# Kernel tuning notes

Measured on AMD Instinct MI355X. Metric: run time of the kernel, lower is better.

## Reference

```python
import jax, jax.numpy as jnp
import numpy as np

N = 50000
E = 1600000
IN_C, HID_C, OUT_C, EDGE_D = 128, 64, 64, 32
NEG_SLOPE = 0.2


def _add_self_loops(edge_index, edge_attr, n):
    # PyG add_self_loops with fill_value='mean': loop attr = mean of incoming edge attrs per node
    src, dst = edge_index[0], edge_index[1]
    attr_sum = jax.ops.segment_sum(edge_attr, dst, num_segments=n)          # [N, D]
    cnt = jax.ops.segment_sum(jnp.ones((edge_attr.shape[0],), edge_attr.dtype), dst, num_segments=n)
    loop_attr = attr_sum / jnp.maximum(cnt, 1.0)[:, None]                   # [N, D]
    loop = jnp.arange(n, dtype=src.dtype)
    src = jnp.concatenate([src, loop])
    dst = jnp.concatenate([dst, loop])
    edge_attr = jnp.concatenate([edge_attr, loop_attr], axis=0)
    return src, dst, edge_attr


def gat_conv(x, edge_index, edge_attr, W, We, att_src, att_dst, att_edge, bias, n):
    # heads=1, concat=True (PyG defaults); att_* have shape [1, C]
    src, dst, ea = _add_self_loops(edge_index, edge_attr, n)
    h = x @ W                                   # [N, C]
    a_src = jnp.sum(h * att_src, axis=-1)       # [N]
    a_dst = jnp.sum(h * att_dst, axis=-1)       # [N]
    he = ea @ We                                # [E+N, C]
    a_edge = jnp.sum(he * att_edge, axis=-1)    # [E+N]
    alpha = a_src[src] + a_dst[dst] + a_edge
    alpha = jax.nn.leaky_relu(alpha, NEG_SLOPE)
    # segment softmax over destination nodes (every node has a self-loop)
    m = jax.ops.segment_max(alpha, dst, num_segments=n)
    alpha = jnp.exp(alpha - m[dst])
    denom = jax.ops.segment_sum(alpha, dst, num_segments=n)
    alpha = alpha / (denom[dst] + 1e-16)
    out = jax.ops.segment_sum(alpha[:, None] * h[src], dst, num_segments=n)  # [N, C]
    return out + bias


def setup_inputs() -> dict:
    key = jax.random.key(0)
    ks = jax.random.split(key, 12)
    def g(k, shape, scale=1.0):
        return jax.random.normal(k, shape, dtype=jnp.float32) * scale
    x = g(ks[0], (N, IN_C))
    edge_index = jax.random.randint(ks[1], (2, E), 0, N, dtype=jnp.int64)
    edge_attr = g(ks[2], (E, EDGE_D))
    s1 = 1.0 / np.sqrt(IN_C)
    s2 = 1.0 / np.sqrt(HID_C)
    se = 1.0 / np.sqrt(EDGE_D)
    return {
        "x": x, "edge_index": edge_index, "edge_attr": edge_attr,
        "W1": g(ks[3], (IN_C, HID_C), s1), "We1": g(ks[4], (EDGE_D, HID_C), se),
        "att_src1": g(ks[5], (1, HID_C), s2), "att_dst1": g(ks[6], (1, HID_C), s2),
        "att_edge1": g(ks[7], (1, HID_C), s2), "b1": jnp.zeros((HID_C,), jnp.float32),
        "W2": g(ks[8], (HID_C, OUT_C), s2), "We2": g(ks[9], (EDGE_D, OUT_C), se),
        "att_src2": g(ks[10], (1, OUT_C), s2), "att_dst2": g(ks[11], (1, OUT_C), s2),
        "att_edge2": g(jax.random.fold_in(key, 99), (1, OUT_C), s2),
        "b2": jnp.zeros((OUT_C,), jnp.float32),
    }


def reference(x, edge_index, edge_attr,
              W1, We1, att_src1, att_dst1, att_edge1, b1,
              W2, We2, att_src2, att_dst2, att_edge2, b2):
    h = gat_conv(x, edge_index, edge_attr, W1, We1, att_src1, att_dst1, att_edge1, b1, N)
    h = jax.nn.relu(h)
    # F.dropout(p=0.1, training=self.training): identity in eval mode
    out = gat_conv(h, edge_index, edge_attr, W2, We2, att_src2, att_dst2, att_edge2, b2, N)
    return out
```

## Files before the change

### kernel.cpp

```cpp
#include <hip/hip_runtime.h>
#include <hip/hip_bf16.h>

__device__ __forceinline__ unsigned f2bf_rne(float f) {
    unsigned u = __float_as_uint(f);
    u += 0x7FFFu + ((u >> 16) & 1u);
    return u >> 16;
}
__device__ __forceinline__ float bf_lo(unsigned p) { return __uint_as_float(p << 16); }
__device__ __forceinline__ float bf_hi(unsigned p) { return __uint_as_float(p & 0xFFFF0000u); }
template <int I> __device__ __forceinline__ float bfsel(unsigned p) {
    return (I == 0) ? bf_lo(p) : bf_hi(p);
}

__global__ __launch_bounds__(256)
void init_kernel(int* __restrict__ cnt, int n,
                 const float* __restrict__ We1, const float* __restrict__ ae1v,
                 const float* __restrict__ We2, const float* __restrict__ ae2v,
                 float* __restrict__ we1, float* __restrict__ we2) {
    int i = blockIdx.x * 256 + threadIdx.x;
    if (i < n) cnt[i] = 0;
    if (blockIdx.x == 0 && threadIdx.x >= 64 && threadIdx.x < 128) {
        int t = threadIdx.x - 64;
        const float* W = (t < 32) ? We1 : We2;
        const float* a = (t < 32) ? ae1v : ae2v;
        float* o       = (t < 32) ? we1 : we2;
        int k = t & 31;
        float s = 0.f;
        for (int c = 0; c < 64; ++c) s += W[k * 64 + c] * a[c];
        o[k] = s;
    }
}

__global__ __launch_bounds__(256)
void edge_pass_kernel(const float4* __restrict__ ea, const int* __restrict__ eidx,
                      const float* __restrict__ we1g, const float* __restrict__ we2g,
                      int* __restrict__ cnt, uint2* __restrict__ pack8,
                      unsigned* __restrict__ meta, int E) {
    int tid = threadIdx.x;
    int q = tid & 7;
    int e = blockIdx.x * 32 + (tid >> 3);
    if (e >= E) return;
    float4 w1 = ((const float4*)we1g)[q];
    float4 w2 = ((const float4*)we2g)[q];
    float4 v = ea[(size_t)e * 8 + q];
    float a1 = v.x * w1.x + v.y * w1.y + v.z * w1.z + v.w * w1.w;
    float a2 = v.x * w2.x + v.y * w2.y + v.z * w2.z + v.w * w2.w;
#pragma unroll
    for (int off = 1; off < 8; off <<= 1) {
        a1 += __shfl_xor(a1, off, 64);
        a2 += __shfl_xor(a2, off, 64);
    }
    if (q == 0) {
        int src = eidx[e];
        int dst = eidx[E + e];
        int rk = atomicAdd(&cnt[dst], 1);
        pack8[e] = make_uint2((unsigned)src, f2bf_rne(a1) | (f2bf_rne(a2) << 16));
        meta[e] = ((unsigned)rk << 16) | (unsigned)dst;
    }
}

__global__ __launch_bounds__(256)
void scanA_kernel(const int* __restrict__ cnt, int* __restrict__ bsum, int n) {
    int idx = blockIdx.x * 256 + threadIdx.x;
    int v = (idx < n) ? cnt[idx] : 0;
#pragma unroll
    for (int off = 32; off >= 1; off >>= 1) v += __shfl_xor(v, off, 64);
    __shared__ int ws[4];
    int lane = threadIdx.x & 63, wid = threadIdx.x >> 6;
    if (lane == 0) ws[wid] = v;
    __syncthreads();
    if (threadIdx.x == 0) bsum[blockIdx.x] = ws[0] + ws[1] + ws[2] + ws[3];
}

__global__ __launch_bounds__(256)
void scanC_kernel(const int* __restrict__ cnt, const int* __restrict__ bsum,
                  int* __restrict__ row_ptr, int n, int E) {
    __shared__ int ws[4];
    __shared__ int woff[4];
    __shared__ int bws[4];
    int lane = threadIdx.x & 63, wid = threadIdx.x >> 6;
    int partial = 0;
    for (int j = threadIdx.x; j < blockIdx.x; j += 256) partial += bsum[j];
#pragma unroll
    for (int off = 32; off >= 1; off >>= 1) partial += __shfl_xor(partial, off, 64);
    if (lane == 0) bws[wid] = partial;
    __syncthreads();
    int boff = bws[0] + bws[1] + bws[2] + bws[3];
    int idx = blockIdx.x * 256 + threadIdx.x;
    int v = (idx < n) ? cnt[idx] : 0;
    int s = v;
#pragma unroll
    for (int off = 1; off < 64; off <<= 1) {
        int t = __shfl_up(s, off, 64);
        if (lane >= off) s += t;
    }
    if (lane == 63) ws[wid] = s;
    __syncthreads();
    if (threadIdx.x == 0) {
        int run = 0;
        for (int w = 0; w < 4; ++w) { int t = ws[w]; woff[w] = run; run += t; }
    }
    __syncthreads();
    if (idx < n) row_ptr[idx] = boff + woff[wid] + s - v;
    if (idx == 0) row_ptr[n] = E;
}

__global__ __launch_bounds__(256)
void scatter_kernel(const uint2* __restrict__ pack8, const unsigned* __restrict__ meta,
                    const int* __restrict__ row_ptr, uint2* __restrict__ s_rec, int E) {
    int e = blockIdx.x * 256 + threadIdx.x;
    if (e >= E) return;
    unsigned m = meta[e];
    int dst = (int)(m & 0xFFFFu);
    int rk  = (int)(m >> 16);
    s_rec[row_ptr[dst] + rk] = pack8[e];
}

template <int INC>
__global__ __launch_bounds__(256)
void gemm_kernel(const float* __restrict__ X, const float* __restrict__ W,
                 const float* __restrict__ asv, const float* __restrict__ adv,
                 __hip_bfloat16* __restrict__ H, float* __restrict__ a_src,
                 float* __restrict__ a_dst, int n) {
    constexpr int LDW = INC + 4;
    __shared__ float Wl[64 * LDW];
    for (int t = threadIdx.x; t < INC * 64; t += 256) {
        int k = t >> 6, c = t & 63;
        Wl[c * LDW + k] = W[t];
    }
    __syncthreads();
    int wid = threadIdx.x >> 6, lane = threadIdx.x & 63;
    int i = blockIdx.x * 4 + wid;
    if (i >= n) return;
    const float4* xr = (const float4*)(X + (size_t)i * INC);
    const float4* wr = (const float4*)(Wl + lane * LDW);
    float acc = 0.f;
#pragma unroll
    for (int k4 = 0; k4 < INC / 4; ++k4) {
        float4 xv = xr[k4];
        float4 wv = wr[k4];
        acc += xv.x * wv.x + xv.y * wv.y + xv.z * wv.z + xv.w * wv.w;
    }
    H[(size_t)i * 64 + lane] = __float2bfloat16(acc);
    float s = acc * asv[lane];
    float d = acc * adv[lane];
#pragma unroll
    for (int off = 32; off >= 1; off >>= 1) {
        s += __shfl_xor(s, off, 64);
        d += __shfl_xor(d, off, 64);
    }
    if (lane == 0) { a_src[i] = s; a_dst[i] = d; }
}

__device__ __forceinline__ float4 bf4_to_f4(ushort4 u) {
    float4 f;
    f.x = __uint_as_float((unsigned)u.x << 16);
    f.y = __uint_as_float((unsigned)u.y << 16);
    f.z = __uint_as_float((unsigned)u.z << 16);
    f.w = __uint_as_float((unsigned)u.w << 16);
    return f;
}

template <int AEIDX, bool RELU, bool FUSE_GEMM2>
__global__ __launch_bounds__(256)
void agg_fused_kernel(const int* __restrict__ row_ptr, const uint2* __restrict__ s_rec,
                      const float* __restrict__ a_srcv, const float* __restrict__ a_dstv,
                      const ushort4* __restrict__ H4, const float* __restrict__ bias,
                      float* __restrict__ out,
                      const float* __restrict__ W2, const float* __restrict__ as2v,
                      const float* __restrict__ ad2v, __hip_bfloat16* __restrict__ H2,
                      float* __restrict__ a_src2, float* __restrict__ a_dst2, int n) {
    __shared__ uint2 wl[4][128];
    __shared__ float4 rowl[4][16];
    int wid = threadIdx.x >> 6, lane = threadIdx.x & 63;
    int i = blockIdx.x * 4 + wid;
    if (i >= n) return;
    int start = row_ptr[i], end = row_ptr[i + 1];
    int deg = end - start;
    float adst = a_dstv[i];

    float w0 = 0.f, w1 = 0.f;
    int src0 = 0, src1 = 0;
    float aeloc = 0.f, dloc = 0.f;
    {
        int j = start + lane;
        if (j < end) {
            uint2 r = s_rec[j];
            float ae = bfsel<AEIDX>(r.y);
            src0 = (int)r.x;
            float a = a_srcv[src0] + adst + ae;
            a = a > 0.f ? a : 0.2f * a;
            w0 = __expf(a);
            aeloc += ae; dloc += w0;
        }
    }
    if (deg > 64) {
        int j = start + 64 + lane;
        if (j < end) {
            uint2 r = s_rec[j];
            float ae = bfsel<AEIDX>(r.y);
            src1 = (int)r.x;
            float a = a_srcv[src1] + adst + ae;
            a = a > 0.f ? a : 0.2f * a;
            w1 = __expf(a);
            aeloc += ae; dloc += w1;
        }
    }
    for (int base = start + 128; base < end; base += 64) {
        int j = base + lane;
        if (j < end) {
            uint2 r = s_rec[j];
            float ae = bfsel<AEIDX>(r.y);
            int s = (int)r.x;
            float a = a_srcv[s] + adst + ae;
            a = a > 0.f ? a : 0.2f * a;
            aeloc += ae; dloc += __expf(a);
        }
    }
#pragma unroll
    for (int off = 32; off >= 1; off >>= 1) {
        aeloc += __shfl_xor(aeloc, off, 64);
        dloc  += __shfl_xor(dloc, off, 64);
    }
    float ael = aeloc / (float)(deg > 0 ? deg : 1);
    float als = a_srcv[i] + adst + ael;
    als = als > 0.f ? als : 0.2f * als;
    float wself = __expf(als);
    float inv = 1.f / (dloc + wself + 1e-16f);

    wl[wid][lane]      = make_uint2((unsigned)src0, __float_as_uint(w0));
    wl[wid][64 + lane] = make_uint2((unsigned)src1, __float_as_uint(w1));

    int sub = lane >> 4;
    int c4  = lane & 15;
    float4 acc = make_float4(0.f, 0.f, 0.f, 0.f);
    int mainCnt = deg < 128 ? deg : 128;
#pragma unroll 4
    for (int r = 0; r < mainCnt; r += 4) {
        uint2 sw = wl[wid][r + sub];
        float w = __uint_as_float(sw.y);
        float4 hv = bf4_to_f4(H4[(size_t)((sw.x << 4) | (unsigned)c4)]);
        acc.x += w * hv.x; acc.y += w * hv.y;
        acc.z += w * hv.z; acc.w += w * hv.w;
    }
    for (int j = start + 128; j < end; j += 4) {
        int jj = j + sub;
        if (jj < end) {
            uint2 r = s_rec[jj];
            float ae = bfsel<AEIDX>(r.y);
            int s = (int)r.x;
            float a = a_srcv[s] + adst + ae;
            a = a > 0.f ? a : 0.2f * a;
            float w = __expf(a);
            float4 hv = bf4_to_f4(H4[(size_t)(((unsigned)s << 4) | (unsigned)c4)]);
            acc.x += w * hv.x; acc.y += w * hv.y;
            acc.z += w * hv.z; acc.w += w * hv.w;
        }
    }
#pragma unroll
    for (int off = 16; off <= 32; off <<= 1) {
        acc.x += __shfl_xor(acc.x, off, 64);
        acc.y += __shfl_xor(acc.y, off, 64);
        acc.z += __shfl_xor(acc.z, off, 64);
        acc.w += __shfl_xor(acc.w, off, 64);
    }
    float4 hv = bf4_to_f4(H4[(size_t)(((unsigned)i << 4) | (unsigned)c4)]);
    float4 bv = ((const float4*)bias)[c4];
    float4 o;
    o.x = (acc.x + wself * hv.x) * inv + bv.x;
    o.y = (acc.y + wself * hv.y) * inv + bv.y;
    o.z = (acc.z + wself * hv.z) * inv + bv.z;
    o.w = (acc.w + wself * hv.w) * inv + bv.w;
    if (RELU) {
        o.x = fmaxf(o.x, 0.f); o.y = fmaxf(o.y, 0.f);
        o.z = fmaxf(o.z, 0.f); o.w = fmaxf(o.w, 0.f);
    }

    if (!FUSE_GEMM2) {
        if (sub == 0) ((float4*)out)[(size_t)i * 16 + c4] = o;
        return;
    }

    if (sub == 0) rowl[wid][c4] = o;
    float acc2 = 0.f;
#pragma unroll
    for (int q = 0; q < 16; ++q) {
        float4 rq = rowl[wid][q];
        acc2 += rq.x * W2[(q * 4 + 0) * 64 + lane];
        acc2 += rq.y * W2[(q * 4 + 1) * 64 + lane];
        acc2 += rq.z * W2[(q * 4 + 2) * 64 + lane];
        acc2 += rq.w * W2[(q * 4 + 3) * 64 + lane];
    }
    H2[(size_t)i * 64 + lane] = __float2bfloat16(acc2);
    float s2 = acc2 * as2v[lane];
    float d2 = acc2 * ad2v[lane];
#pragma unroll
    for (int off = 32; off >= 1; off >>= 1) {
        s2 += __shfl_xor(s2, off, 64);
        d2 += __shfl_xor(d2, off, 64);
    }
    if (lane == 0) { a_src2[i] = s2; a_dst2[i] = d2; }
}

extern "C" void kernel_launch(void* const* d_in, const int* in_sizes, int n_in,
                              void* d_out, int out_size, void* d_ws, size_t ws_size,
                              hipStream_t stream) {
    const float* x        = (const float*)d_in[0];
    const int*   eidx     = (const int*)d_in[1];
    const float* eattr    = (const float*)d_in[2];
    const float* W1       = (const float*)d_in[3];
    const float* We1      = (const float*)d_in[4];
    const float* att_src1 = (const float*)d_in[5];
    const float* att_dst1 = (const float*)d_in[6];
    const float* att_edge1= (const float*)d_in[7];
    const float* b1       = (const float*)d_in[8];
    const float* W2       = (const float*)d_in[9];
    const float* We2      = (const float*)d_in[10];
    const float* att_src2 = (const float*)d_in[11];
    const float* att_dst2 = (const float*)d_in[12];
    const float* att_edge2= (const float*)d_in[13];
    const float* b2       = (const float*)d_in[14];
    float* out = (float*)d_out;

    const int n = in_sizes[0] / 128;
    const int E = in_sizes[1] / 2;

    char* ws = (char*)d_ws;
    size_t off = 0;
    auto carve = [&](size_t bytes) {
        char* p = ws + off;
        off = (off + bytes + 255) & ~(size_t)255;
        return p;
    };
    const int nblkScan = (n + 255) / 256;
    float*    we1    = (float*)carve(32 * 4);
    float*    we2    = (float*)carve(32 * 4);
    int*      cnt    = (int*)carve((size_t)n * 4);
    int*      bsum   = (int*)carve((size_t)nblkScan * 4);
    int*      row_ptr= (int*)carve((size_t)(n + 1) * 4);
    uint2*    pack8  = (uint2*)carve((size_t)E * 8);
    unsigned* meta   = (unsigned*)carve((size_t)E * 4);
    uint2*    s_rec  = (uint2*)carve((size_t)E * 8);
    __hip_bfloat16* bufA = (__hip_bfloat16*)carve((size_t)n * 64 * 2);
    __hip_bfloat16* bufB = (__hip_bfloat16*)carve((size_t)n * 64 * 2);
    float*    a_src  = (float*)carve((size_t)n * 4);
    float*    a_dst  = (float*)carve((size_t)n * 4);
    float*    a_src2 = (float*)carve((size_t)n * 4);
    float*    a_dst2 = (float*)carve((size_t)n * 4);

    init_kernel<<<nblkScan, 256, 0, stream>>>(cnt, n, We1, att_edge1,
                                              We2, att_edge2, we1, we2);

    edge_pass_kernel<<<(E + 31) / 32, 256, 0, stream>>>((const float4*)eattr, eidx,
                                                        we1, we2, cnt, pack8, meta, E);
    scanA_kernel<<<nblkScan, 256, 0, stream>>>(cnt, bsum, n);
    scanC_kernel<<<nblkScan, 256, 0, stream>>>(cnt, bsum, row_ptr, n, E);

    scatter_kernel<<<(E + 255) / 256, 256, 0, stream>>>(pack8, meta, row_ptr, s_rec, E);

    int ngrid = (n + 3) / 4;
    gemm_kernel<128><<<ngrid, 256, 0, stream>>>(x, W1, att_src1, att_dst1,
                                                bufA, a_src, a_dst, n);
    agg_fused_kernel<0, true, true><<<ngrid, 256, 0, stream>>>(
        row_ptr, s_rec, a_src, a_dst, (const ushort4*)bufA, b1,
        nullptr, W2, att_src2, att_dst2, bufB, a_src2, a_dst2, n);
    agg_fused_kernel<1, false, false><<<ngrid, 256, 0, stream>>>(
        row_ptr, s_rec, a_src2, a_dst2, (const ushort4*)bufB, b2,
        out, nullptr, nullptr, nullptr, nullptr, nullptr, nullptr, n);
}
```

Before: 272.7 us.

## Drop meta array, scatter CSR with atomic cursors, transpose W2 for vector loads

The edge pass no longer records each edge's rank or writes a separate meta array. It packs src and dst as 16-bit fields into pack8 and processes two edges per 8-lane group. The scan now also writes a cursor array, and the scatter kernel claims each edge's CSR slot with an atomicAdd on that cursor. This saves a 4-byte-per-edge write and read, at the cost of a returning atomic per edge in scatter and a nondeterministic edge order within each row. W2 is also transposed once in init so the fused second GEMM can use float4 loads per lane instead of scalar column reads.

```diff
diff --git a/kernel.cpp b/kernel.cpp
--- a/kernel.cpp
+++ b/kernel.cpp
@@ -16,7 +16,8 @@
 void init_kernel(int* __restrict__ cnt, int n,
                  const float* __restrict__ We1, const float* __restrict__ ae1v,
                  const float* __restrict__ We2, const float* __restrict__ ae2v,
-                 float* __restrict__ we1, float* __restrict__ we2) {
+                 float* __restrict__ we1, float* __restrict__ we2,
+                 const float* __restrict__ W2, float* __restrict__ W2T) {
     int i = blockIdx.x * 256 + threadIdx.x;
     if (i < n) cnt[i] = 0;
     if (blockIdx.x == 0 && threadIdx.x >= 64 && threadIdx.x < 128) {
@@ -29,33 +30,44 @@
         for (int c = 0; c < 64; ++c) s += W[k * 64 + c] * a[c];
         o[k] = s;
     }
+    if (blockIdx.x == 1) {
+        for (int t = threadIdx.x; t < 4096; t += 256) {
+            int k = t >> 6, c = t & 63;
+            W2T[t] = W2[c * 64 + k];
+        }
+    }
 }
 
 __global__ __launch_bounds__(256)
 void edge_pass_kernel(const float4* __restrict__ ea, const int* __restrict__ eidx,
                       const float* __restrict__ we1g, const float* __restrict__ we2g,
-                      int* __restrict__ cnt, uint2* __restrict__ pack8,
-                      unsigned* __restrict__ meta, int E) {
+                      int* __restrict__ cnt, uint2* __restrict__ pack8, int E) {
     int tid = threadIdx.x;
     int q = tid & 7;
-    int e = blockIdx.x * 32 + (tid >> 3);
-    if (e >= E) return;
+    int slot = tid >> 3;
+    int base = blockIdx.x * 64;
     float4 w1 = ((const float4*)we1g)[q];
     float4 w2 = ((const float4*)we2g)[q];
-    float4 v = ea[(size_t)e * 8 + q];
-    float a1 = v.x * w1.x + v.y * w1.y + v.z * w1.z + v.w * w1.w;
-    float a2 = v.x * w2.x + v.y * w2.y + v.z * w2.z + v.w * w2.w;
-#pragma unroll
-    for (int off = 1; off < 8; off <<= 1) {
-        a1 += __shfl_xor(a1, off, 64);
-        a2 += __shfl_xor(a2, off, 64);
-    }
-    if (q == 0) {
-        int src = eidx[e];
-        int dst = eidx[E + e];
-        int rk = atomicAdd(&cnt[dst], 1);
-        pack8[e] = make_uint2((unsigned)src, f2bf_rne(a1) | (f2bf_rne(a2) << 16));
-        meta[e] = ((unsigned)rk << 16) | (unsigned)dst;
+#pragma unroll
+    for (int h = 0; h < 2; ++h) {
+        int e = base + slot + h * 32;
+        if (e < E) {
+            float4 v = ea[(size_t)e * 8 + q];
+            float a1 = v.x * w1.x + v.y * w1.y + v.z * w1.z + v.w * w1.w;
+            float a2 = v.x * w2.x + v.y * w2.y + v.z * w2.z + v.w * w2.w;
+#pragma unroll
+            for (int off = 1; off < 8; off <<= 1) {
+                a1 += __shfl_xor(a1, off, 64);
+                a2 += __shfl_xor(a2, off, 64);
+            }
+            if (q == 0) {
+                unsigned src = (unsigned)eidx[e];
+                unsigned dst = (unsigned)eidx[E + e];
+                atomicAdd(&cnt[dst], 1);
+                pack8[e] = make_uint2((src << 16) | dst,
+                                      f2bf_rne(a1) | (f2bf_rne(a2) << 16));
+            }
+        }
     }
 }
 
@@ -74,7 +86,7 @@
 
 __global__ __launch_bounds__(256)
 void scanC_kernel(const int* __restrict__ cnt, const int* __restrict__ bsum,
-                  int* __restrict__ row_ptr, int n, int E) {
+                  int* __restrict__ row_ptr, int* __restrict__ cursor, int n, int E) {
     __shared__ int ws[4];
     __shared__ int woff[4];
     __shared__ int bws[4];
@@ -101,19 +113,24 @@
         for (int w = 0; w < 4; ++w) { int t = ws[w]; woff[w] = run; run += t; }
     }
     __syncthreads();
-    if (idx < n) row_ptr[idx] = boff + woff[wid] + s - v;
+    if (idx < n) {
+        int ex = boff + woff[wid] + s - v;
+        row_ptr[idx] = ex;
+        cursor[idx] = ex;
+    }
     if (idx == 0) row_ptr[n] = E;
 }
 
 __global__ __launch_bounds__(256)
-void scatter_kernel(const uint2* __restrict__ pack8, const unsigned* __restrict__ meta,
-                    const int* __restrict__ row_ptr, uint2* __restrict__ s_rec, int E) {
+void scatter_kernel(const uint2* __restrict__ pack8, int* __restrict__ cursor,
+                    uint2* __restrict__ s_rec, int E) {
     int e = blockIdx.x * 256 + threadIdx.x;
     if (e >= E) return;
-    unsigned m = meta[e];
-    int dst = (int)(m & 0xFFFFu);
-    int rk  = (int)(m >> 16);
-    s_rec[row_ptr[dst] + rk] = pack8[e];
+    uint2 p = pack8[e];
+    int dst = (int)(p.x & 0xFFFFu);
+    unsigned src = p.x >> 16;
+    int pos = atomicAdd(&cursor[dst], 1);
+    s_rec[pos] = make_uint2(src, p.y);
 }
 
 template <int INC>
@@ -167,7 +184,7 @@
                       const float* __restrict__ a_srcv, const float* __restrict__ a_dstv,
                       const ushort4* __restrict__ H4, const float* __restrict__ bias,
                       float* __restrict__ out,
-                      const float* __restrict__ W2, const float* __restrict__ as2v,
+                      const float* __restrict__ W2T, const float* __restrict__ as2v,
                       const float* __restrict__ ad2v, __hip_bfloat16* __restrict__ H2,
                       float* __restrict__ a_src2, float* __restrict__ a_dst2, int n) {
     __shared__ uint2 wl[4][128];
@@ -282,14 +299,13 @@
     }
 
     if (sub == 0) rowl[wid][c4] = o;
+    const float4* w2t4 = (const float4*)W2T;
     float acc2 = 0.f;
 #pragma unroll
-    for (int q = 0; q < 16; ++q) {
-        float4 rq = rowl[wid][q];
-        acc2 += rq.x * W2[(q * 4 + 0) * 64 + lane];
-        acc2 += rq.y * W2[(q * 4 + 1) * 64 + lane];
-        acc2 += rq.z * W2[(q * 4 + 2) * 64 + lane];
-        acc2 += rq.w * W2[(q * 4 + 3) * 64 + lane];
+    for (int qq = 0; qq < 16; ++qq) {
+        float4 rq = rowl[wid][qq];
+        float4 wv = w2t4[lane * 16 + qq];
+        acc2 += rq.x * wv.x + rq.y * wv.y + rq.z * wv.z + rq.w * wv.w;
     }
     H2[(size_t)i * 64 + lane] = __float2bfloat16(acc2);
     float s2 = acc2 * as2v[lane];
@@ -335,11 +351,12 @@
     const int nblkScan = (n + 255) / 256;
     float*    we1    = (float*)carve(32 * 4);
     float*    we2    = (float*)carve(32 * 4);
+    float*    W2T    = (float*)carve(64 * 64 * 4);
     int*      cnt    = (int*)carve((size_t)n * 4);
     int*      bsum   = (int*)carve((size_t)nblkScan * 4);
     int*      row_ptr= (int*)carve((size_t)(n + 1) * 4);
+    int*      cursor = (int*)carve((size_t)n * 4);
     uint2*    pack8  = (uint2*)carve((size_t)E * 8);
-    unsigned* meta   = (unsigned*)carve((size_t)E * 4);
     uint2*    s_rec  = (uint2*)carve((size_t)E * 8);
     __hip_bfloat16* bufA = (__hip_bfloat16*)carve((size_t)n * 64 * 2);
     __hip_bfloat16* bufB = (__hip_bfloat16*)carve((size_t)n * 64 * 2);
@@ -349,21 +366,21 @@
     float*    a_dst2 = (float*)carve((size_t)n * 4);
 
     init_kernel<<<nblkScan, 256, 0, stream>>>(cnt, n, We1, att_edge1,
-                                              We2, att_edge2, we1, we2);
-
-    edge_pass_kernel<<<(E + 31) / 32, 256, 0, stream>>>((const float4*)eattr, eidx,
-                                                        we1, we2, cnt, pack8, meta, E);
+                                              We2, att_edge2, we1, we2, W2, W2T);
+
+    edge_pass_kernel<<<(E + 63) / 64, 256, 0, stream>>>((const float4*)eattr, eidx,
+                                                        we1, we2, cnt, pack8, E);
     scanA_kernel<<<nblkScan, 256, 0, stream>>>(cnt, bsum, n);
-    scanC_kernel<<<nblkScan, 256, 0, stream>>>(cnt, bsum, row_ptr, n, E);
-
-    scatter_kernel<<<(E + 255) / 256, 256, 0, stream>>>(pack8, meta, row_ptr, s_rec, E);
+    scanC_kernel<<<nblkScan, 256, 0, stream>>>(cnt, bsum, row_ptr, cursor, n, E);
+
+    scatter_kernel<<<(E + 255) / 256, 256, 0, stream>>>(pack8, cursor, s_rec, E);
 
     int ngrid = (n + 3) / 4;
     gemm_kernel<128><<<ngrid, 256, 0, stream>>>(x, W1, att_src1, att_dst1,
                                                 bufA, a_src, a_dst, n);
     agg_fused_kernel<0, true, true><<<ngrid, 256, 0, stream>>>(
         row_ptr, s_rec, a_src, a_dst, (const ushort4*)bufA, b1,
-        nullptr, W2, att_src2, att_dst2, bufB, a_src2, a_dst2, n);
+        nullptr, W2T, att_src2, att_dst2, bufB, a_src2, a_dst2, n);
     agg_fused_kernel<1, false, false><<<ngrid, 256, 0, stream>>>(
         row_ptr, s_rec, a_src2, a_dst2, (const ushort4*)bufB, b2,
         out, nullptr, nullptr, nullptr, nullptr, nullptr, nullptr, n);
```

After: 427.8 us. 56.9% more time.
